# Optimization experiments

Measured on AMD Instinct MI355X. Metric: run time of the kernel, lower is better.

Reference implementation:

```python
import jax, jax.numpy as jnp
import numpy as np

HIDDEN = 64
CHANNELS = [256, 256, 256]
SHAPES = [(4, 256, 128, 128), (4, 256, 64, 64), (4, 256, 32, 32)]


def setup_inputs() -> dict:
    key = jax.random.key(0)
    ks = jax.random.split(key, 16)
    d = {}
    for i, shp in enumerate(SHAPES):
        d[f"x{i}"] = jax.random.normal(ks[i], shp, dtype=jnp.float32)
    kidx = 3
    for i, c in enumerate(CHANNELS):
        # convs1: 1x1 conv c -> HIDDEN (stored as [c_in, c_out] matrix)
        d[f"W1_{i}"] = jax.random.normal(ks[kidx], (c, HIDDEN), dtype=jnp.float32) * (1.0 / np.sqrt(c)); kidx += 1
        d[f"b1_{i}"] = jnp.zeros((HIDDEN,), dtype=jnp.float32)
        # convs2: 1x1 conv (HIDDEN + HIDDEN//2) -> c
        cin2 = HIDDEN + HIDDEN // 2
        d[f"W2_{i}"] = jax.random.normal(ks[kidx], (cin2, c), dtype=jnp.float32) * (1.0 / np.sqrt(cin2)); kidx += 1
        d[f"b2_{i}"] = jnp.zeros((c,), dtype=jnp.float32)
    return d


def _conv1x1(x, W, b):
    # x: [B, Cin, H, W], W: [Cin, Cout] -> [B, Cout, H, W]
    return jnp.einsum("bchw,cd->bdhw", x, W) + b[None, :, None, None]


def _level(x, W1, b1, W2, b2):
    y = _conv1x1(x, W1, b1)                      # [B, HIDDEN, H, W]
    out, fmap = jnp.split(y, 2, axis=1)          # each [B, HIDDEN//2, H, W]
    z = jnp.concatenate([out, fmap, jax.nn.relu(fmap)], axis=1)  # [B, 1.5*HIDDEN, H, W]
    return _conv1x1(z, W2, b2)                   # [B, Cin, H, W]


def reference(x0, x1, x2,
              W1_0, b1_0, W2_0, b2_0,
              W1_1, b1_1, W2_1, b2_1,
              W1_2, b1_2, W2_2, b2_2):
    o0 = _level(x0, W1_0, b1_0, W2_0, b2_0)
    o1 = _level(x1, W1_1, b1_1, W2_1, b2_1)
    o2 = _level(x2, W1_2, b1_2, W2_2, b2_2)
    return (o0, o1, o2)
```

## Files before the change

kernel.cpp:

```cpp
#include <hip/hip_runtime.h>

typedef __attribute__((ext_vector_type(8))) short short8;
typedef __attribute__((ext_vector_type(4))) float float4v;

__device__ __forceinline__ unsigned short f2bf(float f) {
    unsigned u = __float_as_uint(f);
    u = (u + 0x7FFFu + ((u >> 16) & 1u)) >> 16;
    return (unsigned short)u;
}

#define XSET 520
#define CROW 68
#define CS_BYTES 34816
#define ZS_BYTES 12480

__global__ void prepack(const float* __restrict__ W1_0, const float* __restrict__ W2_0,
                        const float* __restrict__ W1_1, const float* __restrict__ W2_1,
                        const float* __restrict__ W1_2, const float* __restrict__ W2_2,
                        unsigned short* __restrict__ ws) {
    int e = blockIdx.x * 256 + threadIdx.x;
    if (e >= 3 * 40960) return;
    int l = e / 40960, r = e % 40960;
    const float* W1 = (l == 0) ? W1_0 : (l == 1) ? W1_1 : W1_2;
    const float* W2 = (l == 0) ? W2_0 : (l == 1) ? W2_1 : W2_2;
    unsigned short* base = ws + l * 40960;
    if (r < 16384) {
        int j = r & 7, lane = (r >> 3) & 63, fs = r >> 9;
        int mt = fs >> 3, ks = fs & 7;
        int k = ks * 32 + (lane >> 4) * 8 + j;
        int m = mt * 16 + (lane & 15);
        base[r] = f2bf(W1[k * 64 + m]);
    } else {
        int r2 = r - 16384;
        int j = r2 & 7, lane = (r2 >> 3) & 63, fs = r2 >> 9;
        int mt = fs / 3, ks = fs - mt * 3;
        int k = ks * 32 + (lane >> 4) * 8 + j;
        int m = mt * 16 + (lane & 15);
        base[16384 + r2] = f2bf(W2[k * 256 + m]);
    }
}

template<int HW>
__device__ __forceinline__ void level3(
    const float* __restrict__ x,
    const unsigned short* __restrict__ A1,
    const unsigned short* __restrict__ A2,
    const float* __restrict__ b1, const float* __restrict__ b2,
    float* __restrict__ o, int px0,
    unsigned short* __restrict__ xs,
    unsigned short* __restrict__ zs)
{
    const int t = (int)threadIdx.x;
    const int lane = t & 63, w = t >> 6;
    const int q = lane >> 4, n = lane & 15;

    {
        const int ch_lo = t >> 4;
        const int pp = t & 15;
        const int g = pp >> 2;
        const int n0 = (pp & 3) * 4;
        const float* xp = x + (size_t)ch_lo * HW + px0 + 4 * pp;
#pragma unroll
        for (int i = 0; i < 16; ++i) {
            const int ch = i * 16 + ch_lo;
            float4v v = *(const float4v*)(xp + (size_t)i * 16 * HW);
            const int ks = ch >> 5, qq = (ch >> 3) & 3, j = ch & 7;
            unsigned short* base = xs + (g * 8 + ks) * XSET + j;
#pragma unroll
            for (int e = 0; e < 4; ++e)
                base[(qq * 16 + n0 + e) * 8] = f2bf(v[e]);
        }
    }
    __syncthreads();

    float4v acc1[4];
#pragma unroll
    for (int mt = 0; mt < 4; ++mt)
        acc1[mt] = *(const float4v*)(b1 + mt * 16 + q * 4);

    short8 xf[8];
#pragma unroll
    for (int ks = 0; ks < 8; ++ks)
        xf[ks] = *(const short8*)(xs + (w * 8 + ks) * XSET + lane * 8);

    const short8* A1f = (const short8*)A1;
#pragma unroll
    for (int ks = 0; ks < 8; ++ks)
#pragma unroll
        for (int mt = 0; mt < 4; ++mt)
            acc1[mt] = __builtin_amdgcn_mfma_f32_16x16x32_bf16(
                A1f[(mt * 8 + ks) * 64 + lane], xf[ks], acc1[mt], 0, 0, 0);

    {
        unsigned short* zg = zs + w * 3 * XSET;
#pragma unroll
        for (int mt = 0; mt < 4; ++mt) {
            const int kb = mt * 16 + q * 4;
            unsigned long long pk =
                  (unsigned long long)f2bf(acc1[mt][0])
                | ((unsigned long long)f2bf(acc1[mt][1]) << 16)
                | ((unsigned long long)f2bf(acc1[mt][2]) << 32)
                | ((unsigned long long)f2bf(acc1[mt][3]) << 48);
            *(unsigned long long*)(zg + (kb >> 5) * XSET +
                (((kb >> 3) & 3) * 16 + n) * 8 + (kb & 7)) = pk;
            if (mt >= 2) {
                const int kr = kb + 32;
                unsigned long long pr =
                      (unsigned long long)f2bf(fmaxf(acc1[mt][0], 0.f))
                    | ((unsigned long long)f2bf(fmaxf(acc1[mt][1], 0.f)) << 16)
                    | ((unsigned long long)f2bf(fmaxf(acc1[mt][2], 0.f)) << 32)
                    | ((unsigned long long)f2bf(fmaxf(acc1[mt][3], 0.f)) << 48);
                *(unsigned long long*)(zg + (kr >> 5) * XSET +
                    (((kr >> 3) & 3) * 16 + n) * 8 + (kr & 7)) = pr;
            }
        }
    }
    __syncthreads();

    float4v acc2[4][4];
#pragma unroll
    for (int mm = 0; mm < 4; ++mm) {
        float4v bb = *(const float4v*)(b2 + (w * 4 + mm) * 16 + q * 4);
#pragma unroll
        for (int g = 0; g < 4; ++g) acc2[mm][g] = bb;
    }

    const short8* A2f = (const short8*)A2;
#pragma unroll
    for (int g = 0; g < 4; ++g) {
        short8 zf[3];
#pragma unroll
        for (int ks = 0; ks < 3; ++ks)
            zf[ks] = *(const short8*)(zs + (g * 3 + ks) * XSET + lane * 8);
#pragma unroll
        for (int ks = 0; ks < 3; ++ks)
#pragma unroll
            for (int mm = 0; mm < 4; ++mm)
                acc2[mm][g] = __builtin_amdgcn_mfma_f32_16x16x32_bf16(
                    A2f[((w * 4 + mm) * 3 + ks) * 64 + lane], zf[ks], acc2[mm][g], 0, 0, 0);
    }

    float* cw = (float*)xs + w * 32 * CROW;
#pragma unroll
    for (int p = 0; p < 2; ++p) {
#pragma unroll
        for (int mp = 0; mp < 2; ++mp) {
            const int mm = p * 2 + mp;
#pragma unroll
            for (int g = 0; g < 4; ++g)
#pragma unroll
                for (int r = 0; r < 4; ++r)
                    cw[(mp * 16 + q * 4 + r) * CROW + g * 16 + n] = acc2[mm][g][r];
        }
        const int chs = lane >> 4;
        const int pp = lane & 15;
        float* op = o + (size_t)(w * 64 + p * 32 + chs) * HW + px0 + 4 * pp;
#pragma unroll
        for (int i = 0; i < 8; ++i) {
            float4v v = *(const float4v*)(cw + (i * 4 + chs) * CROW + 4 * pp);
            __builtin_nontemporal_store(v, (float4v*)(op + (size_t)(i * 4) * HW));
        }
    }
}

__global__ __launch_bounds__(256, 3) void fused_v3(
    const float* __restrict__ x0, const float* __restrict__ x1, const float* __restrict__ x2,
    const float* __restrict__ b1_0, const float* __restrict__ b2_0,
    const float* __restrict__ b1_1, const float* __restrict__ b2_1,
    const float* __restrict__ b1_2, const float* __restrict__ b2_2,
    const unsigned short* __restrict__ wpk, float* __restrict__ out)
{
    __shared__ __align__(16) unsigned char smem[CS_BYTES + ZS_BYTES];
    unsigned short* xs = (unsigned short*)smem;
    unsigned short* zs = (unsigned short*)(smem + CS_BYTES);
    const int bi = (int)blockIdx.x;

    if (bi < 1024) {
        int b = bi >> 8, px0 = (bi & 255) * 64;
        level3<16384>(x0 + (size_t)b * 256 * 16384, wpk, wpk + 16384, b1_0, b2_0,
                      out + (size_t)b * 256 * 16384, px0, xs, zs);
    } else if (bi < 1280) {
        int r = bi - 1024, b = r >> 6, px0 = (r & 63) * 64;
        level3<4096>(x1 + (size_t)b * 256 * 4096, wpk + 40960, wpk + 40960 + 16384,
                     b1_1, b2_1, out + 16777216 + (size_t)b * 256 * 4096, px0, xs, zs);
    } else {
        int r = bi - 1280, b = r >> 4, px0 = (r & 15) * 64;
        level3<1024>(x2 + (size_t)b * 256 * 1024, wpk + 81920, wpk + 81920 + 16384,
                     b1_2, b2_2, out + 20971520 + (size_t)b * 256 * 1024, px0, xs, zs);
    }
}

extern "C" void kernel_launch(void* const* d_in, const int* in_sizes, int n_in,
                              void* d_out, int out_size, void* d_ws, size_t ws_size,
                              hipStream_t stream) {
    const float* x0   = (const float*)d_in[0];
    const float* x1   = (const float*)d_in[1];
    const float* x2   = (const float*)d_in[2];
    const float* W1_0 = (const float*)d_in[3];
    const float* b1_0 = (const float*)d_in[4];
    const float* W2_0 = (const float*)d_in[5];
    const float* b2_0 = (const float*)d_in[6];
    const float* W1_1 = (const float*)d_in[7];
    const float* b1_1 = (const float*)d_in[8];
    const float* W2_1 = (const float*)d_in[9];
    const float* b2_1 = (const float*)d_in[10];
    const float* W1_2 = (const float*)d_in[11];
    const float* b1_2 = (const float*)d_in[12];
    const float* W2_2 = (const float*)d_in[13];
    const float* b2_2 = (const float*)d_in[14];
    float* out = (float*)d_out;
    unsigned short* wpk = (unsigned short*)d_ws;

    prepack<<<dim3(480), dim3(256), 0, stream>>>(W1_0, W2_0, W1_1, W2_1, W1_2, W2_2, wpk);
    fused_v3<<<dim3(1344), dim3(256), 0, stream>>>(
        x0, x1, x2, b1_0, b2_0, b1_1, b2_1, b1_2, b2_2, wpk, out);
}
```

Before: 190.6 us.

## Alias z buffer onto x staging LDS and batch input loads for higher occupancy

Removes the separate z-staging LDS region by reusing the x staging buffer, adding barriers so phases don't overlap, which lowers per-block LDS and raises launch bounds to 4 blocks per CU. Input loads are hoisted into a 16-element register array so all global loads are issued before the bf16 conversion stores. A per-group offset is added to the LDS x layout to spread bank accesses. The extra barriers and larger register footprint may limit the occupancy gain or add stalls.

```diff
diff --git a/kernel.cpp b/kernel.cpp
--- a/kernel.cpp
+++ b/kernel.cpp
@@ -11,8 +11,7 @@
 
 #define XSET 520
 #define CROW 68
-#define CS_BYTES 34816
-#define ZS_BYTES 12480
+#define SMEM_BYTES 34816
 
 __global__ void prepack(const float* __restrict__ W1_0, const float* __restrict__ W2_0,
                         const float* __restrict__ W1_1, const float* __restrict__ W2_1,
@@ -47,12 +46,12 @@
     const unsigned short* __restrict__ A2,
     const float* __restrict__ b1, const float* __restrict__ b2,
     float* __restrict__ o, int px0,
-    unsigned short* __restrict__ xs,
-    unsigned short* __restrict__ zs)
+    unsigned short* __restrict__ xs)
 {
     const int t = (int)threadIdx.x;
     const int lane = t & 63, w = t >> 6;
     const int q = lane >> 4, n = lane & 15;
+    unsigned short* zs = xs;
 
     {
         const int ch_lo = t >> 4;
@@ -60,15 +59,18 @@
         const int g = pp >> 2;
         const int n0 = (pp & 3) * 4;
         const float* xp = x + (size_t)ch_lo * HW + px0 + 4 * pp;
+        float4v v[16];
+#pragma unroll
+        for (int i = 0; i < 16; ++i)
+            v[i] = *(const float4v*)(xp + (size_t)(i * 16) * HW);
 #pragma unroll
         for (int i = 0; i < 16; ++i) {
             const int ch = i * 16 + ch_lo;
-            float4v v = *(const float4v*)(xp + (size_t)i * 16 * HW);
             const int ks = ch >> 5, qq = (ch >> 3) & 3, j = ch & 7;
-            unsigned short* base = xs + (g * 8 + ks) * XSET + j;
+            unsigned short* base = xs + (g * 8 + ks) * XSET + g * 8 + j;
 #pragma unroll
             for (int e = 0; e < 4; ++e)
-                base[(qq * 16 + n0 + e) * 8] = f2bf(v[e]);
+                base[(qq * 16 + n0 + e) * 8] = f2bf(v[i][e]);
         }
     }
     __syncthreads();
@@ -81,7 +83,8 @@
     short8 xf[8];
 #pragma unroll
     for (int ks = 0; ks < 8; ++ks)
-        xf[ks] = *(const short8*)(xs + (w * 8 + ks) * XSET + lane * 8);
+        xf[ks] = *(const short8*)(xs + (w * 8 + ks) * XSET + w * 8 + lane * 8);
+    __syncthreads();
 
     const short8* A1f = (const short8*)A1;
 #pragma unroll
@@ -139,6 +142,7 @@
                 acc2[mm][g] = __builtin_amdgcn_mfma_f32_16x16x32_bf16(
                     A2f[((w * 4 + mm) * 3 + ks) * 64 + lane], zf[ks], acc2[mm][g], 0, 0, 0);
     }
+    __syncthreads();
 
     float* cw = (float*)xs + w * 32 * CROW;
 #pragma unroll
@@ -163,30 +167,29 @@
     }
 }
 
-__global__ __launch_bounds__(256, 3) void fused_v3(
+__global__ __launch_bounds__(256, 4) void fused_v5(
     const float* __restrict__ x0, const float* __restrict__ x1, const float* __restrict__ x2,
     const float* __restrict__ b1_0, const float* __restrict__ b2_0,
     const float* __restrict__ b1_1, const float* __restrict__ b2_1,
     const float* __restrict__ b1_2, const float* __restrict__ b2_2,
     const unsigned short* __restrict__ wpk, float* __restrict__ out)
 {
-    __shared__ __align__(16) unsigned char smem[CS_BYTES + ZS_BYTES];
+    __shared__ __align__(16) unsigned char smem[SMEM_BYTES];
     unsigned short* xs = (unsigned short*)smem;
-    unsigned short* zs = (unsigned short*)(smem + CS_BYTES);
     const int bi = (int)blockIdx.x;
 
     if (bi < 1024) {
         int b = bi >> 8, px0 = (bi & 255) * 64;
         level3<16384>(x0 + (size_t)b * 256 * 16384, wpk, wpk + 16384, b1_0, b2_0,
-                      out + (size_t)b * 256 * 16384, px0, xs, zs);
+                      out + (size_t)b * 256 * 16384, px0, xs);
     } else if (bi < 1280) {
         int r = bi - 1024, b = r >> 6, px0 = (r & 63) * 64;
         level3<4096>(x1 + (size_t)b * 256 * 4096, wpk + 40960, wpk + 40960 + 16384,
-                     b1_1, b2_1, out + 16777216 + (size_t)b * 256 * 4096, px0, xs, zs);
+                     b1_1, b2_1, out + 16777216 + (size_t)b * 256 * 4096, px0, xs);
     } else {
         int r = bi - 1280, b = r >> 4, px0 = (r & 15) * 64;
         level3<1024>(x2 + (size_t)b * 256 * 1024, wpk + 81920, wpk + 81920 + 16384,
-                     b1_2, b2_2, out + 20971520 + (size_t)b * 256 * 1024, px0, xs, zs);
+                     b1_2, b2_2, out + 20971520 + (size_t)b * 256 * 1024, px0, xs);
     }
 }
 
@@ -212,6 +215,6 @@
     unsigned short* wpk = (unsigned short*)d_ws;
 
     prepack<<<dim3(480), dim3(256), 0, stream>>>(W1_0, W2_0, W1_1, W2_1, W1_2, W2_2, wpk);
-    fused_v3<<<dim3(1344), dim3(256), 0, stream>>>(
+    fused_v5<<<dim3(1344), dim3(256), 0, stream>>>(
         x0, x1, x2, b1_0, b2_0, b1_1, b2_1, b1_2, b2_2, wpk, out);
 }
```

New measurement: 196.8 us. 3.3% more time.
